# Optimization experiments

Measured on AMD Instinct MI355X. Metric: run time of the kernel, lower is better.

Reference implementation:

```python
import jax, jax.numpy as jnp
import numpy as np

B, H, S, D = 2, 16, 2048, 64

def setup_inputs() -> dict:
    key = jax.random.key(0)
    kq, kk, kv, km = jax.random.split(key, 4)
    q = jax.random.normal(kq, (B, H, S, D), dtype=jnp.float32)
    k = jax.random.normal(kk, (B, H, S, D), dtype=jnp.float32)
    v = jax.random.normal(kv, (B, H, S, D), dtype=jnp.float32)
    mask = jax.random.randint(km, (1, 1, S, S), 0, 2, dtype=jnp.int32)
    return {"q": q, "k": k, "v": v, "mask": mask}

def reference(q, k, v, mask):
    d_k = q.shape[-1]
    # scores: [B,H,S,S] = q @ k^T / sqrt(d_k)
    scores = jnp.einsum('bhqd,bhkd->bhqk', q, k) / jnp.sqrt(jnp.float32(d_k))
    scores = jnp.where(mask == 0, -jnp.inf, scores)
    score = jax.nn.softmax(scores, axis=-1)
    output = jnp.einsum('bhqk,bhkd->bhqd', score, v)
    return (output, score)
```

## Files before the change

kernel.cpp:

```cpp
#include <hip/hip_runtime.h>
#include <hip/hip_bf16.h>


#define BH 32
#define SEQ 2048
#define DIM 64

typedef __attribute__((ext_vector_type(8))) short short8;
typedef __attribute__((ext_vector_type(4))) float floatx4;

__device__ __forceinline__ short f2bf(float f) {
    unsigned u = __builtin_bit_cast(unsigned, f);
    unsigned r = u + 0x7fffu + ((u >> 16) & 1u);
    return (short)(r >> 16);
}

__device__ __forceinline__ short8 cvt_frag(float4 a, float4 b) {
    short8 r;
    r[0] = f2bf(a.x); r[1] = f2bf(a.y); r[2] = f2bf(a.z); r[3] = f2bf(a.w);
    r[4] = f2bf(b.x); r[5] = f2bf(b.y); r[6] = f2bf(b.z); r[7] = f2bf(b.w);
    return r;
}

__device__ __forceinline__ short8 load_frag_f32(const float* p) {
    float4 a = *reinterpret_cast<const float4*>(p);
    float4 b = *reinterpret_cast<const float4*>(p + 4);
    return cvt_frag(a, b);
}


__global__ void maskbits_kernel(const int* __restrict__ mask,
                                unsigned long long* __restrict__ bits) {
    int tid = blockIdx.x * blockDim.x + threadIdx.x;
    unsigned long long b = __ballot(mask[tid] != 0);
    if ((threadIdx.x & 63) == 0) bits[tid >> 6] = b;
}

__global__ void cvt_k_kernel(const float* __restrict__ k, short* __restrict__ kb) {
    size_t i = ((size_t)blockIdx.x * blockDim.x + threadIdx.x) * 8;
    float4 a = *reinterpret_cast<const float4*>(k + i);
    float4 b = *reinterpret_cast<const float4*>(k + i + 4);
    *reinterpret_cast<short8*>(kb + i) = cvt_frag(a, b);
}

__global__ __launch_bounds__(256) void cvt_vt_kernel(const float* __restrict__ v,
                                                     short* __restrict__ vt) {
    __shared__ float tile[64][65];
    const int bh = blockIdx.y;
    const int sblk = blockIdx.x;
    const int t = threadIdx.x;
    const float* vb = v + ((size_t)bh * SEQ + sblk * 64) * DIM;
#pragma unroll
    for (int it = 0; it < 4; ++it) {
        int row = it * 16 + (t >> 4);
        int c4 = (t & 15) * 4;
        float4 a = *reinterpret_cast<const float4*>(vb + row * DIM + c4);
        tile[row][c4] = a.x; tile[row][c4 + 1] = a.y;
        tile[row][c4 + 2] = a.z; tile[row][c4 + 3] = a.w;
    }
    __syncthreads();
    short* vo = vt + (size_t)bh * SEQ * DIM;
#pragma unroll
    for (int it = 0; it < 2; ++it) {
        int c = it * 256 + t;
        int d = c >> 3;
        int s8 = (c & 7) * 8;
        short8 r;
#pragma unroll
        for (int j = 0; j < 8; ++j) r[j] = f2bf(tile[s8 + j][d]);
        *reinterpret_cast<short8*>(vo + (size_t)d * SEQ + sblk * 64 + s8) = r;
    }
}


__global__ __launch_bounds__(256) void attn_fast(
    const float* __restrict__ q, const short* __restrict__ kb,
    const short* __restrict__ vt, const unsigned int* __restrict__ maskbits,
    float* __restrict__ out, float* __restrict__ score)
{
    __shared__ float plds[4][16][33];

    const int bh   = blockIdx.y;
    const int qb   = blockIdx.x;
    const int wave = threadIdx.x >> 6;
    const int lane = threadIdx.x & 63;
    const int quad = lane >> 4;
    const int n    = lane & 15;
    const int q0   = qb * 64 + wave * 16;

    const float* qbase = q  + (size_t)bh * SEQ * DIM;
    const short* kbb   = kb + (size_t)bh * SEQ * DIM;
    const short* vtb   = vt + (size_t)bh * SEQ * DIM;

    const short8 qf0 = load_frag_f32(qbase + (size_t)(q0 + n) * DIM + quad * 8);
    const short8 qf1 = load_frag_f32(qbase + (size_t)(q0 + n) * DIM + 32 + quad * 8);

    const short* kn  = kbb + (size_t)n * DIM + quad * 8;
    const short* vn0 = vtb + (size_t)n * SEQ + quad * 8;
    const unsigned int* mrp[4];
    float* srp[4];
    float* srow = score + (size_t)bh * SEQ * SEQ;
#pragma unroll
    for (int r = 0; r < 4; ++r) {
        const int row = q0 + quad * 4 + r;
        mrp[r] = maskbits + (size_t)row * (SEQ / 32);
        srp[r] = srow + (size_t)row * SEQ + n;
    }

    float l[4] = {0.f, 0.f, 0.f, 0.f};
    for (int cp = 0; cp < SEQ / 32; ++cp) {
        const int cbase = cp * 32;
        const short* k0 = kn + (size_t)cbase * DIM;
        short8 kf00 = *reinterpret_cast<const short8*>(k0);
        short8 kf01 = *reinterpret_cast<const short8*>(k0 + 32);
        short8 kf10 = *reinterpret_cast<const short8*>(k0 + 16 * DIM);
        short8 kf11 = *reinterpret_cast<const short8*>(k0 + 16 * DIM + 32);
        floatx4 a0 = {0.f, 0.f, 0.f, 0.f}, a1 = {0.f, 0.f, 0.f, 0.f};
        a0 = __builtin_amdgcn_mfma_f32_16x16x32_bf16(qf0, kf00, a0, 0, 0, 0);
        a0 = __builtin_amdgcn_mfma_f32_16x16x32_bf16(qf1, kf01, a0, 0, 0, 0);
        a1 = __builtin_amdgcn_mfma_f32_16x16x32_bf16(qf0, kf10, a1, 0, 0, 0);
        a1 = __builtin_amdgcn_mfma_f32_16x16x32_bf16(qf1, kf11, a1, 0, 0, 0);
#pragma unroll
        for (int r = 0; r < 4; ++r) {
            const unsigned w = mrp[r][cp];
            float e0 = ((w >> n) & 1u)        ? __expf(a0[r] * 0.125f) : 0.f;
            float e1 = ((w >> (n + 16)) & 1u) ? __expf(a1[r] * 0.125f) : 0.f;
            l[r] += e0 + e1;
        }
    }
#pragma unroll
    for (int r = 0; r < 4; ++r) {
        float x = l[r];
        x += __shfl_xor(x, 1, 64);
        x += __shfl_xor(x, 2, 64);
        x += __shfl_xor(x, 4, 64);
        x += __shfl_xor(x, 8, 64);
        l[r] = 1.0f / x;
    }

    floatx4 o[4];
#pragma unroll
    for (int t = 0; t < 4; ++t) o[t] = (floatx4){0.f, 0.f, 0.f, 0.f};

    for (int cp = 0; cp < SEQ / 32; ++cp) {
        const int cbase = cp * 32;
        const short* k0 = kn + (size_t)cbase * DIM;
        short8 kf00 = *reinterpret_cast<const short8*>(k0);
        short8 kf01 = *reinterpret_cast<const short8*>(k0 + 32);
        short8 kf10 = *reinterpret_cast<const short8*>(k0 + 16 * DIM);
        short8 kf11 = *reinterpret_cast<const short8*>(k0 + 16 * DIM + 32);
        floatx4 a0 = {0.f, 0.f, 0.f, 0.f}, a1 = {0.f, 0.f, 0.f, 0.f};
        a0 = __builtin_amdgcn_mfma_f32_16x16x32_bf16(qf0, kf00, a0, 0, 0, 0);
        a0 = __builtin_amdgcn_mfma_f32_16x16x32_bf16(qf1, kf01, a0, 0, 0, 0);
        a1 = __builtin_amdgcn_mfma_f32_16x16x32_bf16(qf0, kf10, a1, 0, 0, 0);
        a1 = __builtin_amdgcn_mfma_f32_16x16x32_bf16(qf1, kf11, a1, 0, 0, 0);

#pragma unroll
        for (int r = 0; r < 4; ++r) {
            const unsigned w = mrp[r][cp];
            float e0 = ((w >> n) & 1u)        ? __expf(a0[r] * 0.125f) : 0.f;
            float e1 = ((w >> (n + 16)) & 1u) ? __expf(a1[r] * 0.125f) : 0.f;
            float p0 = e0 * l[r];
            float p1 = e1 * l[r];
            srp[r][cbase]      = p0;
            srp[r][cbase + 16] = p1;
            plds[wave][quad * 4 + r][n]      = p0;
            plds[wave][quad * 4 + r][n + 16] = p1;
        }
        __builtin_amdgcn_wave_barrier();
        short8 pf;
#pragma unroll
        for (int j = 0; j < 8; ++j) pf[j] = f2bf(plds[wave][n][quad * 8 + j]);
        __builtin_amdgcn_wave_barrier();

#pragma unroll
        for (int t = 0; t < 4; ++t) {
            short8 vf = *reinterpret_cast<const short8*>(vn0 + (size_t)t * 16 * SEQ + cbase);
            o[t] = __builtin_amdgcn_mfma_f32_16x16x32_bf16(pf, vf, o[t], 0, 0, 0);
        }
    }

    float* obase = out + ((size_t)bh * SEQ + q0) * DIM;
#pragma unroll
    for (int t = 0; t < 4; ++t)
#pragma unroll
        for (int r = 0; r < 4; ++r)
            obase[(size_t)(quad * 4 + r) * DIM + t * 16 + n] = o[t][r];
}


__global__ __launch_bounds__(256) void attn_ref(
    const float* __restrict__ q, const float* __restrict__ k,
    const float* __restrict__ v, const int* __restrict__ mask,
    const unsigned int* __restrict__ maskbits, int use_bits,
    float* __restrict__ out, float* __restrict__ score)
{
    __shared__ float plds[4][16][36];
    const int bh   = blockIdx.y;
    const int qb   = blockIdx.x;
    const int wave = threadIdx.x >> 6;
    const int lane = threadIdx.x & 63;
    const int quad = lane >> 4;
    const int n    = lane & 15;
    const int q0   = qb * 64 + wave * 16;
    const float* qbase = q + (size_t)bh * SEQ * DIM;
    const float* kbase = k + (size_t)bh * SEQ * DIM;
    const float* vbase = v + (size_t)bh * SEQ * DIM;
    const short8 qf0 = load_frag_f32(qbase + (size_t)(q0 + n) * DIM + quad * 8);
    const short8 qf1 = load_frag_f32(qbase + (size_t)(q0 + n) * DIM + 32 + quad * 8);
    float l[4] = {0.f, 0.f, 0.f, 0.f};
    for (int ct = 0; ct < SEQ / 16; ++ct) {
        const int col0 = ct * 16;
        short8 kf0 = load_frag_f32(kbase + (size_t)(col0 + n) * DIM + quad * 8);
        short8 kf1 = load_frag_f32(kbase + (size_t)(col0 + n) * DIM + 32 + quad * 8);
        floatx4 acc = {0.f, 0.f, 0.f, 0.f};
        acc = __builtin_amdgcn_mfma_f32_16x16x32_bf16(qf0, kf0, acc, 0, 0, 0);
        acc = __builtin_amdgcn_mfma_f32_16x16x32_bf16(qf1, kf1, acc, 0, 0, 0);
#pragma unroll
        for (int r = 0; r < 4; ++r) {
            const int row = q0 + quad * 4 + r;
            int mbit;
            if (use_bits) {
                unsigned w = maskbits[((size_t)row * SEQ + col0) >> 5];
                mbit = (w >> ((col0 & 31) + n)) & 1;
            } else {
                mbit = (mask[(size_t)row * SEQ + col0 + n] != 0);
            }
            l[r] += mbit ? __expf(acc[r] * 0.125f) : 0.0f;
        }
    }
#pragma unroll
    for (int r = 0; r < 4; ++r) {
        float x = l[r];
        x += __shfl_xor(x, 1, 64);
        x += __shfl_xor(x, 2, 64);
        x += __shfl_xor(x, 4, 64);
        x += __shfl_xor(x, 8, 64);
        l[r] = 1.0f / x;
    }
    floatx4 o[4];
#pragma unroll
    for (int t = 0; t < 4; ++t) o[t] = (floatx4){0.f, 0.f, 0.f, 0.f};
    float* srow = score + (size_t)bh * SEQ * SEQ;
    for (int cp = 0; cp < SEQ / 32; ++cp) {
        const int cbase = cp * 32;
#pragma unroll
        for (int half = 0; half < 2; ++half) {
            const int col0 = cbase + half * 16;
            short8 kf0 = load_frag_f32(kbase + (size_t)(col0 + n) * DIM + quad * 8);
            short8 kf1 = load_frag_f32(kbase + (size_t)(col0 + n) * DIM + 32 + quad * 8);
            floatx4 acc = {0.f, 0.f, 0.f, 0.f};
            acc = __builtin_amdgcn_mfma_f32_16x16x32_bf16(qf0, kf0, acc, 0, 0, 0);
            acc = __builtin_amdgcn_mfma_f32_16x16x32_bf16(qf1, kf1, acc, 0, 0, 0);
#pragma unroll
            for (int r = 0; r < 4; ++r) {
                const int row = q0 + quad * 4 + r;
                int mbit;
                if (use_bits) {
                    unsigned w = maskbits[((size_t)row * SEQ + col0) >> 5];
                    mbit = (w >> ((col0 & 31) + n)) & 1;
                } else {
                    mbit = (mask[(size_t)row * SEQ + col0 + n] != 0);
                }
                float e = mbit ? __expf(acc[r] * 0.125f) : 0.0f;
                float p = e * l[r];
                srow[(size_t)row * SEQ + col0 + n] = p;
                plds[wave][quad * 4 + r][half * 16 + n] = p;
            }
        }
        short8 pf = load_frag_f32(&plds[wave][n][quad * 8]);
#pragma unroll
        for (int t = 0; t < 4; ++t) {
            short8 vf;
#pragma unroll
            for (int j = 0; j < 8; ++j)
                vf[j] = f2bf(vbase[(size_t)(cbase + quad * 8 + j) * DIM + t * 16 + n]);
            o[t] = __builtin_amdgcn_mfma_f32_16x16x32_bf16(pf, vf, o[t], 0, 0, 0);
        }
    }
    float* obase = out + ((size_t)bh * SEQ + q0) * DIM;
#pragma unroll
    for (int t = 0; t < 4; ++t)
#pragma unroll
        for (int r = 0; r < 4; ++r)
            obase[(size_t)(quad * 4 + r) * DIM + t * 16 + n] = o[t][r];
}


extern "C" void kernel_launch(void* const* d_in, const int* in_sizes, int n_in,
                              void* d_out, int out_size, void* d_ws, size_t ws_size,
                              hipStream_t stream) {
    const float* q    = (const float*)d_in[0];
    const float* k    = (const float*)d_in[1];
    const float* v    = (const float*)d_in[2];
    const int*   mask = (const int*)d_in[3];

    float* out   = (float*)d_out;
    float* score = out + (size_t)BH * SEQ * DIM;

    const size_t bits_bytes = (size_t)SEQ * SEQ / 8;
    const size_t kb_bytes   = (size_t)BH * SEQ * DIM * 2;
    const size_t need_fast  = bits_bytes + 2 * kb_bytes;

    dim3 grid(SEQ / 64, BH);

    if (ws_size >= need_fast) {
        unsigned long long* bits = (unsigned long long*)d_ws;
        short* kbuf = (short*)((char*)d_ws + bits_bytes);
        short* vtb  = (short*)((char*)d_ws + bits_bytes + kb_bytes);

        maskbits_kernel<<<(SEQ * SEQ) / 256, 256, 0, stream>>>(mask, bits);
        cvt_k_kernel<<<(BH * SEQ * DIM / 8) / 256, 256, 0, stream>>>(k, kbuf);
        cvt_vt_kernel<<<dim3(SEQ / 64, BH), 256, 0, stream>>>(v, vtb);

        attn_fast<<<grid, 256, 0, stream>>>(q, kbuf, vtb,
                                            (const unsigned int*)d_ws, out, score);
    } else {
        const int use_bits = (ws_size >= bits_bytes) ? 1 : 0;
        if (use_bits)
            maskbits_kernel<<<(SEQ * SEQ) / 256, 256, 0, stream>>>(
                mask, (unsigned long long*)d_ws);
        attn_ref<<<grid, 256, 0, stream>>>(q, k, v, mask,
                                           (const unsigned int*)d_ws, use_bits,
                                           out, score);
    }
}
```

Measured before the change: 909.9 us.

## Split key range across wave pairs, transpose QK^T to avoid LDS P reshuffle

Each block now covers 32 query rows, and pairs of waves split the key sequence in half. Partial row sums are exchanged through shared memory, and the output partials are combined through shared memory at the end. QK^T is computed transposed so each lane holds one query row, which allows one mask word per iteration and float4 score stores. The P fragment for the PV MFMA is built with permlane swaps instead of an LDS round-trip. This doubles grid parallelism and cuts LDS traffic, at the cost of extra block syncs and a reduction through shared memory.

```diff
diff --git a/kernel.cpp b/kernel.cpp
--- a/kernel.cpp
+++ b/kernel.cpp
@@ -8,11 +8,20 @@
 
 typedef __attribute__((ext_vector_type(8))) short short8;
 typedef __attribute__((ext_vector_type(4))) float floatx4;
+typedef __attribute__((ext_vector_type(4))) unsigned int uintx4;
 
 __device__ __forceinline__ short f2bf(float f) {
     unsigned u = __builtin_bit_cast(unsigned, f);
     unsigned r = u + 0x7fffu + ((u >> 16) & 1u);
     return (short)(r >> 16);
+}
+
+__device__ __forceinline__ unsigned pack2bf(float lo, float hi) {
+    unsigned ul = __builtin_bit_cast(unsigned, lo);
+    unsigned uh = __builtin_bit_cast(unsigned, hi);
+    ul = ul + 0x7fffu + ((ul >> 16) & 1u);
+    uh = uh + 0x7fffu + ((uh >> 16) & 1u);
+    return (ul >> 16) | (uh & 0xffff0000u);
 }
 
 __device__ __forceinline__ short8 cvt_frag(float4 a, float4 b) {
@@ -73,12 +82,13 @@
 }
 
 
-__global__ __launch_bounds__(256) void attn_fast(
+__global__ __launch_bounds__(256, 8) void attn_fast(
     const float* __restrict__ q, const short* __restrict__ kb,
     const short* __restrict__ vt, const unsigned int* __restrict__ maskbits,
     float* __restrict__ out, float* __restrict__ score)
 {
-    __shared__ float plds[4][16][33];
+    __shared__ float lpart[4][16];
+    __shared__ float ocomb[2][4][4][64];
 
     const int bh   = blockIdx.y;
     const int qb   = blockIdx.x;
@@ -86,7 +96,11 @@
     const int lane = threadIdx.x & 63;
     const int quad = lane >> 4;
     const int n    = lane & 15;
-    const int q0   = qb * 64 + wave * 16;
+    const int half = wave & 1;
+    const int q0   = qb * 32 + (wave >> 1) * 16;
+    const int q4   = quad * 4;
+    const int cp0  = half * (SEQ / 64);
+    const int cp1  = cp0 + (SEQ / 64);
 
     const float* qbase = q  + (size_t)bh * SEQ * DIM;
     const short* kbb   = kb + (size_t)bh * SEQ * DIM;
@@ -97,18 +111,11 @@
 
     const short* kn  = kbb + (size_t)n * DIM + quad * 8;
     const short* vn0 = vtb + (size_t)n * SEQ + quad * 8;
-    const unsigned int* mrp[4];
-    float* srp[4];
-    float* srow = score + (size_t)bh * SEQ * SEQ;
-#pragma unroll
-    for (int r = 0; r < 4; ++r) {
-        const int row = q0 + quad * 4 + r;
-        mrp[r] = maskbits + (size_t)row * (SEQ / 32);
-        srp[r] = srow + (size_t)row * SEQ + n;
-    }
-
-    float l[4] = {0.f, 0.f, 0.f, 0.f};
-    for (int cp = 0; cp < SEQ / 32; ++cp) {
+    const unsigned int* mr = maskbits + (size_t)(q0 + n) * (SEQ / 32);
+    float* sb = score + (size_t)bh * SEQ * SEQ + (size_t)(q0 + n) * SEQ + q4;
+
+    float lsum = 0.f;
+    for (int cp = cp0; cp < cp1; ++cp) {
         const int cbase = cp * 32;
         const short* k0 = kn + (size_t)cbase * DIM;
         short8 kf00 = *reinterpret_cast<const short8*>(k0);
@@ -116,33 +123,29 @@
         short8 kf10 = *reinterpret_cast<const short8*>(k0 + 16 * DIM);
         short8 kf11 = *reinterpret_cast<const short8*>(k0 + 16 * DIM + 32);
         floatx4 a0 = {0.f, 0.f, 0.f, 0.f}, a1 = {0.f, 0.f, 0.f, 0.f};
-        a0 = __builtin_amdgcn_mfma_f32_16x16x32_bf16(qf0, kf00, a0, 0, 0, 0);
-        a0 = __builtin_amdgcn_mfma_f32_16x16x32_bf16(qf1, kf01, a0, 0, 0, 0);
-        a1 = __builtin_amdgcn_mfma_f32_16x16x32_bf16(qf0, kf10, a1, 0, 0, 0);
-        a1 = __builtin_amdgcn_mfma_f32_16x16x32_bf16(qf1, kf11, a1, 0, 0, 0);
+        a0 = __builtin_amdgcn_mfma_f32_16x16x32_bf16(kf00, qf0, a0, 0, 0, 0);
+        a0 = __builtin_amdgcn_mfma_f32_16x16x32_bf16(kf01, qf1, a0, 0, 0, 0);
+        a1 = __builtin_amdgcn_mfma_f32_16x16x32_bf16(kf10, qf0, a1, 0, 0, 0);
+        a1 = __builtin_amdgcn_mfma_f32_16x16x32_bf16(kf11, qf1, a1, 0, 0, 0);
+        const unsigned w = mr[cp];
 #pragma unroll
         for (int r = 0; r < 4; ++r) {
-            const unsigned w = mrp[r][cp];
-            float e0 = ((w >> n) & 1u)        ? __expf(a0[r] * 0.125f) : 0.f;
-            float e1 = ((w >> (n + 16)) & 1u) ? __expf(a1[r] * 0.125f) : 0.f;
-            l[r] += e0 + e1;
-        }
-    }
-#pragma unroll
-    for (int r = 0; r < 4; ++r) {
-        float x = l[r];
-        x += __shfl_xor(x, 1, 64);
-        x += __shfl_xor(x, 2, 64);
-        x += __shfl_xor(x, 4, 64);
-        x += __shfl_xor(x, 8, 64);
-        l[r] = 1.0f / x;
-    }
+            float e0 = ((w >> (q4 + r)) & 1u)      ? __expf(a0[r] * 0.125f) : 0.f;
+            float e1 = ((w >> (q4 + r + 16)) & 1u) ? __expf(a1[r] * 0.125f) : 0.f;
+            lsum += e0 + e1;
+        }
+    }
+    lsum += __shfl_xor(lsum, 16, 64);
+    lsum += __shfl_xor(lsum, 32, 64);
+    if (lane < 16) lpart[wave][lane] = lsum;
+    __syncthreads();
+    const float invl = 1.0f / (lsum + lpart[wave ^ 1][n]);
 
     floatx4 o[4];
 #pragma unroll
     for (int t = 0; t < 4; ++t) o[t] = (floatx4){0.f, 0.f, 0.f, 0.f};
 
-    for (int cp = 0; cp < SEQ / 32; ++cp) {
+    for (int cp = cp0; cp < cp1; ++cp) {
         const int cbase = cp * 32;
         const short* k0 = kn + (size_t)cbase * DIM;
         short8 kf00 = *reinterpret_cast<const short8*>(k0);
@@ -150,28 +153,32 @@
         short8 kf10 = *reinterpret_cast<const short8*>(k0 + 16 * DIM);
         short8 kf11 = *reinterpret_cast<const short8*>(k0 + 16 * DIM + 32);
         floatx4 a0 = {0.f, 0.f, 0.f, 0.f}, a1 = {0.f, 0.f, 0.f, 0.f};
-        a0 = __builtin_amdgcn_mfma_f32_16x16x32_bf16(qf0, kf00, a0, 0, 0, 0);
-        a0 = __builtin_amdgcn_mfma_f32_16x16x32_bf16(qf1, kf01, a0, 0, 0, 0);
-        a1 = __builtin_amdgcn_mfma_f32_16x16x32_bf16(qf0, kf10, a1, 0, 0, 0);
-        a1 = __builtin_amdgcn_mfma_f32_16x16x32_bf16(qf1, kf11, a1, 0, 0, 0);
-
+        a0 = __builtin_amdgcn_mfma_f32_16x16x32_bf16(kf00, qf0, a0, 0, 0, 0);
+        a0 = __builtin_amdgcn_mfma_f32_16x16x32_bf16(kf01, qf1, a0, 0, 0, 0);
+        a1 = __builtin_amdgcn_mfma_f32_16x16x32_bf16(kf10, qf0, a1, 0, 0, 0);
+        a1 = __builtin_amdgcn_mfma_f32_16x16x32_bf16(kf11, qf1, a1, 0, 0, 0);
+        const unsigned w = mr[cp];
+        float p0[4], p1[4];
 #pragma unroll
         for (int r = 0; r < 4; ++r) {
-            const unsigned w = mrp[r][cp];
-            float e0 = ((w >> n) & 1u)        ? __expf(a0[r] * 0.125f) : 0.f;
-            float e1 = ((w >> (n + 16)) & 1u) ? __expf(a1[r] * 0.125f) : 0.f;
-            float p0 = e0 * l[r];
-            float p1 = e1 * l[r];
-            srp[r][cbase]      = p0;
-            srp[r][cbase + 16] = p1;
-            plds[wave][quad * 4 + r][n]      = p0;
-            plds[wave][quad * 4 + r][n + 16] = p1;
-        }
-        __builtin_amdgcn_wave_barrier();
-        short8 pf;
-#pragma unroll
-        for (int j = 0; j < 8; ++j) pf[j] = f2bf(plds[wave][n][quad * 8 + j]);
-        __builtin_amdgcn_wave_barrier();
+            float e0 = ((w >> (q4 + r)) & 1u)      ? __expf(a0[r] * 0.125f) : 0.f;
+            float e1 = ((w >> (q4 + r + 16)) & 1u) ? __expf(a1[r] * 0.125f) : 0.f;
+            p0[r] = e0 * invl;
+            p1[r] = e1 * invl;
+        }
+        *reinterpret_cast<float4*>(sb + cbase)      = make_float4(p0[0], p0[1], p0[2], p0[3]);
+        *reinterpret_cast<float4*>(sb + cbase + 16) = make_float4(p1[0], p1[1], p1[2], p1[3]);
+
+        unsigned a0L = pack2bf(p0[0], p0[1]);
+        unsigned a0H = pack2bf(p0[2], p0[3]);
+        unsigned a1L = pack2bf(p1[0], p1[1]);
+        unsigned a1H = pack2bf(p1[2], p1[3]);
+        asm("v_permlane32_swap_b32 %0, %1" : "+v"(a0L), "+v"(a1L));
+        asm("v_permlane16_swap_b32 %0, %1" : "+v"(a0L), "+v"(a1L));
+        asm("v_permlane32_swap_b32 %0, %1" : "+v"(a0H), "+v"(a1H));
+        asm("v_permlane16_swap_b32 %0, %1" : "+v"(a0H), "+v"(a1H));
+        uintx4 pu = {a0L, a0H, a1L, a1H};
+        short8 pf = __builtin_bit_cast(short8, pu);
 
 #pragma unroll
         for (int t = 0; t < 4; ++t) {
@@ -180,12 +187,23 @@
         }
     }
 
-    float* obase = out + ((size_t)bh * SEQ + q0) * DIM;
-#pragma unroll
-    for (int t = 0; t < 4; ++t)
-#pragma unroll
-        for (int r = 0; r < 4; ++r)
-            obase[(size_t)(quad * 4 + r) * DIM + t * 16 + n] = o[t][r];
+    if (half) {
+#pragma unroll
+        for (int t = 0; t < 4; ++t)
+#pragma unroll
+            for (int r = 0; r < 4; ++r)
+                ocomb[wave >> 1][t][r][lane] = o[t][r];
+    }
+    __syncthreads();
+    if (!half) {
+        float* obase = out + ((size_t)bh * SEQ + q0) * DIM;
+#pragma unroll
+        for (int t = 0; t < 4; ++t)
+#pragma unroll
+            for (int r = 0; r < 4; ++r)
+                obase[(size_t)(quad * 4 + r) * DIM + t * 16 + n] =
+                    o[t][r] + ocomb[wave >> 1][t][r][lane];
+    }
 }
 
 
@@ -302,8 +320,6 @@
     const size_t kb_bytes   = (size_t)BH * SEQ * DIM * 2;
     const size_t need_fast  = bits_bytes + 2 * kb_bytes;
 
-    dim3 grid(SEQ / 64, BH);
-
     if (ws_size >= need_fast) {
         unsigned long long* bits = (unsigned long long*)d_ws;
         short* kbuf = (short*)((char*)d_ws + bits_bytes);
@@ -313,6 +329,7 @@
         cvt_k_kernel<<<(BH * SEQ * DIM / 8) / 256, 256, 0, stream>>>(k, kbuf);
         cvt_vt_kernel<<<dim3(SEQ / 64, BH), 256, 0, stream>>>(v, vtb);
 
+        dim3 grid(SEQ / 32, BH);
         attn_fast<<<grid, 256, 0, stream>>>(q, kbuf, vtb,
                                             (const unsigned int*)d_ws, out, score);
     } else {
@@ -320,6 +337,7 @@
         if (use_bits)
             maskbits_kernel<<<(SEQ * SEQ) / 256, 256, 0, stream>>>(
                 mask, (unsigned long long*)d_ws);
+        dim3 grid(SEQ / 64, BH);
         attn_ref<<<grid, 256, 0, stream>>>(q, k, v, mask,
                                            (const unsigned int*)d_ws, use_bits,
                                            out, score);
```

New measurement: 929.4 us. 2.1% more time.
